# Optimization experiments

Hardware: AMD Instinct MI355X
Metric: run time of the kernel (lower is better)

The kernel has to match this reference:

```python
import jax, jax.numpy as jnp
import numpy as np

HEADS = 8
EPS = 1e-6
LN_EPS = 1e-5


def avg_pool(x, k):
    b, c, h, w = x.shape
    return x.reshape(b, c, h // k, k, w // k, k).mean(axis=(3, 5))


def layernorm(x, g, b):
    mu = x.mean(-1, keepdims=True)
    var = x.var(-1, keepdims=True)
    return (x - mu) / jnp.sqrt(var + LN_EPS) * g + b


def pos_embed_2d(h, w, c):
    # original calls build_2d_sincos_position_embedding(w=h, h=w): grid over (h, w), row-major flatten
    gw, gh = jnp.meshgrid(jnp.arange(h, dtype=jnp.float32),
                          jnp.arange(w, dtype=jnp.float32), indexing='ij')
    pd = c // 4
    omega = 1.0 / (10000.0 ** (jnp.arange(pd, dtype=jnp.float32) / pd))
    ow = gw.reshape(-1, 1) * omega  # (h*w, pd)
    oh = gh.reshape(-1, 1) * omega
    return jnp.concatenate([jnp.sin(ow), jnp.cos(ow), jnp.sin(oh), jnp.cos(oh)], axis=1)  # (h*w, c)


def _forward(a3, a4, q_w, q_b, q_ln_g, q_ln_b, k_w, k_b, k_ln_g, k_ln_b,
             v_w, v_b, out_w, out_b, lin1_w, lin1_b, lin2_w, lin2_b,
             n1_g, n1_b, n2_g, n2_b, idx):
    orig_a3 = a3
    if idx == 2:
        a3d = avg_pool(a3, 2)
    else:
        a3d = avg_pool(a3, 4)
        a4 = avg_pool(a4, 2)
    bs, c, h, w = a3d.shape
    L = h * w  # tgt_len == src_len (a3_down and a4 have equal spatial size)
    hd = c // HEADS

    residual = a3d.reshape(bs, c, L).transpose(0, 2, 1)  # (b, L, c)
    x3 = residual
    x4 = a4.reshape(bs, c, L).transpose(0, 2, 1)
    pos = pos_embed_2d(h, w, c)  # (L, c)
    x3 = x3 + pos[None]
    x4 = x4 + pos[None]

    Q = layernorm(x3 @ q_w + q_b, q_ln_g, q_ln_b)
    K = layernorm(x4 @ k_w + k_b, k_ln_g, k_ln_b)
    V = x4 @ v_w + v_b
    Q = jax.nn.relu(Q).reshape(bs, L, HEADS, hd).transpose(0, 2, 1, 3)  # (b,h,L,d)
    K = jax.nn.relu(K).reshape(bs, L, HEADS, hd).transpose(0, 2, 1, 3)
    V = V.reshape(bs, L, HEADS, hd).transpose(0, 2, 1, 3)

    # cosFormer position reweighting: index = pi/2 * (1..m) / m
    m = L
    wi = (np.pi / 2.0) * jnp.arange(1, m + 1, dtype=jnp.float32) / m  # (m,)
    sn = jnp.sin(wi)[None, None, :, None]
    cs = jnp.cos(wi)[None, None, :, None]
    Q_ = jnp.concatenate([Q * sn, Q * cs], axis=-1)  # (b,h,L,2d)
    K_ = jnp.concatenate([K * sn, K * cs], axis=-1)

    KV = jnp.einsum('bhld,bhlm->bhdm', K_, V)                     # (b,h,2d,d)
    Z = 1.0 / jnp.maximum(jnp.einsum('bhld,bhd->bhl', Q_, K_.sum(axis=2)), EPS)
    attn = jnp.einsum('bhld,bhdm->bhlm', Q_, KV) * Z[..., None]   # (b,h,L,d)
    attn = attn.transpose(0, 2, 1, 3).reshape(bs, L, c)

    out = attn @ out_w + out_b
    out = layernorm(out, n1_g, n1_b)     # normalize_before=False -> norm1 applied
    out = residual + out                 # dropout=0
    res2 = out
    out = jax.nn.gelu(out @ lin1_w + lin1_b, approximate=False) @ lin2_w + lin2_b
    out = layernorm(out, n2_g, n2_b)
    out = res2 + out

    a3sa = out.transpose(0, 2, 1).reshape(bs, c, h, w)
    a3sa = jax.image.resize(a3sa, orig_a3.shape, method='bilinear')  # align_corners=False
    return a3sa * orig_a3


def setup_inputs() -> dict:
    key = jax.random.key(0)
    ks = jax.random.split(key, 10)
    B, C = 16, 256
    C4 = 4 * C

    def w(k, shp):
        return jax.random.normal(k, shp, dtype=jnp.float32) * 0.02

    return {
        'a3': jax.random.normal(ks[0], (B, C, 128, 128), dtype=jnp.float32),
        'a4': jax.random.normal(ks[1], (B, C, 64, 64), dtype=jnp.float32),
        'q_w': w(ks[2], (C, C)), 'q_b': jnp.zeros((C,), jnp.float32),
        'q_ln_g': jnp.ones((C,), jnp.float32), 'q_ln_b': jnp.zeros((C,), jnp.float32),
        'k_w': w(ks[3], (C, C)), 'k_b': jnp.zeros((C,), jnp.float32),
        'k_ln_g': jnp.ones((C,), jnp.float32), 'k_ln_b': jnp.zeros((C,), jnp.float32),
        'v_w': w(ks[4], (C, C)), 'v_b': jnp.zeros((C,), jnp.float32),
        'out_w': w(ks[5], (C, C)), 'out_b': jnp.zeros((C,), jnp.float32),
        'lin1_w': w(ks[6], (C, C4)), 'lin1_b': jnp.zeros((C4,), jnp.float32),
        'lin2_w': w(ks[7], (C4, C)), 'lin2_b': jnp.zeros((C,), jnp.float32),
        'n1_g': jnp.ones((C,), jnp.float32), 'n1_b': jnp.zeros((C,), jnp.float32),
        'n2_g': jnp.ones((C,), jnp.float32), 'n2_b': jnp.zeros((C,), jnp.float32),
        'idx': 2,
    }


def reference(a3, a4, q_w, q_b, q_ln_g, q_ln_b, k_w, k_b, k_ln_g, k_ln_b,
              v_w, v_b, out_w, out_b, lin1_w, lin1_b, lin2_w, lin2_b,
              n1_g, n1_b, n2_g, n2_b, idx):
    return _forward(a3, a4, q_w, q_b, q_ln_g, q_ln_b, k_w, k_b, k_ln_g, k_ln_b,
                    v_w, v_b, out_w, out_b, lin1_w, lin1_b, lin2_w, lin2_b,
                    n1_g, n1_b, n2_g, n2_b, idx)
```

## Files before the change

kernel.cpp:

```cpp
#include <hip/hip_runtime.h>
#include <hip/hip_bf16.h>
#include <math.h>

#define HEADS 8
#define LL 4096
#define CDIM 256
#define BATCH 16
#define NROWS (BATCH*LL)

typedef __attribute__((ext_vector_type(8))) __bf16 bf16x8;
typedef __attribute__((ext_vector_type(4))) float f32x4;

__device__ inline float b2f(ushort u) {
    union { unsigned u; float f; } v; v.u = ((unsigned)u) << 16; return v.f;
}
__device__ inline ushort f2b(float f) {
    union { float f; unsigned u; } v; v.f = f;
    unsigned r = (v.u + 0x7FFF + ((v.u >> 16) & 1)) >> 16;
    return (ushort)r;
}
__device__ inline void gload16(const void* g, void* l) {
    __builtin_amdgcn_global_load_lds(
        (const __attribute__((address_space(1))) unsigned int*)g,
        (__attribute__((address_space(3))) unsigned int*)l, 16, 0, 0);
}

__global__ __launch_bounds__(256) void prep_kernel(
    float* __restrict__ pos, float* __restrict__ snc,
    const float* __restrict__ q_w, const float* __restrict__ k_w,
    const float* __restrict__ v_w, const float* __restrict__ o_w,
    const float* __restrict__ w1, const float* __restrict__ w2,
    ushort* __restrict__ wqT, ushort* __restrict__ wkT,
    ushort* __restrict__ wvT, ushort* __restrict__ woT,
    ushort* __restrict__ w1T, ushort* __restrict__ w2T)
{
    __shared__ float t[32][33];
    int bid = blockIdx.x;
    int tid = threadIdx.x;
    if (bid < 1024) {
        int c = tid;
        int k = c & 63;
        float omega = expf(-(float)k * (9.210340371976184f / 64.0f));
        #pragma unroll
        for (int i = 0; i < 4; ++i) {
            int l = bid * 4 + i;
            int y = l >> 6, x = l & 63;
            float coord = (c < 128) ? (float)y : (float)x;
            float ang = coord * omega;
            float val = ((c & 127) < 64) ? sinf(ang) : cosf(ang);
            pos[l * CDIM + c] = val;
            if (c < 2) {
                float wi = 1.5707963267948966f * (float)(l + 1) / (float)LL;
                snc[l * 2 + c] = (c == 0) ? sinf(wi) : cosf(wi);
            }
        }
        return;
    }
    int id = bid - 1024;
    const float* W; ushort* Wt; int K, N, kb, nb;
    if (id < 64)       { W = q_w; Wt = wqT; K = 256;  N = 256;  kb = (id & 7) * 32;  nb = (id >> 3) * 32; }
    else if (id < 128) { id -= 64;  W = k_w; Wt = wkT; K = 256;  N = 256;  kb = (id & 7) * 32;  nb = (id >> 3) * 32; }
    else if (id < 192) { id -= 128; W = v_w; Wt = wvT; K = 256;  N = 256;  kb = (id & 7) * 32;  nb = (id >> 3) * 32; }
    else if (id < 256) { id -= 192; W = o_w; Wt = woT; K = 256;  N = 256;  kb = (id & 7) * 32;  nb = (id >> 3) * 32; }
    else if (id < 512) { id -= 256; W = w1;  Wt = w1T; K = 256;  N = 1024; kb = (id & 7) * 32;  nb = (id >> 3) * 32; }
    else               { id -= 512; W = w2;  Wt = w2T; K = 1024; N = 256;  kb = (id & 31) * 32; nb = (id >> 5) * 32; }
    int x = tid & 31, y = tid >> 5;
    #pragma unroll
    for (int i = 0; i < 4; ++i)
        t[y + i * 8][x] = W[(size_t)(kb + y + i * 8) * N + nb + x];
    __syncthreads();
    #pragma unroll
    for (int i = 0; i < 4; ++i) {
        int n = y + i * 8;
        Wt[(size_t)(nb + n) * K + kb + x] = f2b(t[x][n]);
    }
}

__global__ __launch_bounds__(256) void pool_x3_kernel(
    const float* __restrict__ a3, ushort* __restrict__ residual,
    ushort* __restrict__ x3b, const float* __restrict__ pos)
{
    __shared__ float raw[64][128];
    __shared__ float pooled[64][65];
    int i = blockIdx.x, ct = blockIdx.y, b = blockIdx.z;
    int tid = threadIdx.x;
    #pragma unroll
    for (int it = 0; it < 8; ++it) {
        int lin = (it * 256 + tid) * 4;
        int x = lin & 127;
        int cc = lin >> 7;
        size_t base = ((size_t)(b * 256 + ct * 64 + cc) * 128 + 2 * i) * 128 + x;
        float4 v0 = *(const float4*)&a3[base];
        float4 v1 = *(const float4*)&a3[base + 128];
        float4 s = make_float4(v0.x + v1.x, v0.y + v1.y, v0.z + v1.z, v0.w + v1.w);
        *(float4*)&raw[cc][x] = s;
    }
    __syncthreads();
    #pragma unroll
    for (int it = 0; it < 16; ++it) {
        int idx = it * 256 + tid;
        int j = idx & 63, cc = idx >> 6;
        pooled[cc][j] = 0.25f * (raw[cc][2 * j] + raw[cc][2 * j + 1]);
    }
    __syncthreads();
    #pragma unroll
    for (int it = 0; it < 16; ++it) {
        int cc = tid & 63;
        int jj = (tid >> 6) + it * 4;
        float val = pooled[cc][jj];
        int l = i * 64 + jj;
        int c = ct * 64 + cc;
        size_t o = (size_t)(b * LL + l) * CDIM + c;
        residual[o] = f2b(val);
        x3b[o] = f2b(val + pos[l * CDIM + c]);
    }
}

__global__ __launch_bounds__(256) void x4_kernel(
    const float* __restrict__ a4, ushort* __restrict__ x4b, const float* __restrict__ pos)
{
    __shared__ float t2[64][65];
    int y = blockIdx.x, ct = blockIdx.y, b = blockIdx.z, tid = threadIdx.x;
    #pragma unroll
    for (int it = 0; it < 16; ++it) {
        int idx = it * 256 + tid;
        int x = idx & 63, cc = idx >> 6;
        t2[cc][x] = a4[((size_t)(b * 256 + ct * 64 + cc) * 64 + y) * 64 + x];
    }
    __syncthreads();
    #pragma unroll
    for (int it = 0; it < 16; ++it) {
        int cc = tid & 63;
        int xx = (tid >> 6) + it * 4;
        int l = y * 64 + xx, c = ct * 64 + cc;
        x4b[(size_t)(b * LL + l) * CDIM + c] = f2b(t2[cc][xx] + pos[l * CDIM + c]);
    }
}

template<bool DO_LN, bool DO_RELU, bool DO_GELU, bool DO_RES>
__global__ __launch_bounds__(512, 2) void gemm_mfma(
    const ushort* __restrict__ A, const ushort* __restrict__ Wt,
    const float* __restrict__ bias, const float* __restrict__ gam_,
    const float* __restrict__ bet_, const ushort* __restrict__ res,
    ushort* __restrict__ outb, int K, int colsTot)
{
    __shared__ ushort As[128 * 32];
    __shared__ ushort Bs[256 * 32];
    __shared__ float redS[128][4];
    __shared__ float redQ[128][4];
    __shared__ float2 mustd[128];

    const int tid = threadIdx.x;
    const int lane = tid & 63;
    const int wv = tid >> 6;
    const int wr = wv >> 2;
    const int wc = wv & 3;
    const int wvu = __builtin_amdgcn_readfirstlane(wv);
    const int row0 = blockIdx.x * 128;
    const int cb = blockIdx.y * 256;

    const int sr = tid >> 2;
    const int sg = (tid & 3) ^ ((sr >> 1) & 3);
    const ushort* aSrc = A + (size_t)(row0 + sr) * K + sg * 8;
    const ushort* bSrc0 = Wt + (size_t)(cb + sr) * K + sg * 8;
    const ushort* bSrc1 = Wt + (size_t)(cb + 128 + sr) * K + sg * 8;

    const int frSlot = (lane >> 4) ^ (((lane & 15) >> 1) & 3);

    f32x4 acc[4][4] = {};
    for (int kb = 0; kb < K; kb += 32) {
        gload16(aSrc + kb, (char*)&As[0] + wvu * 1024);
        gload16(bSrc0 + kb, (char*)&Bs[0] + wvu * 1024);
        gload16(bSrc1 + kb, (char*)&Bs[0] + 8192 + wvu * 1024);
        __syncthreads();

        bf16x8 af[4], bfr[4];
        #pragma unroll
        for (int f = 0; f < 4; ++f) {
            int r = wr * 64 + f * 16 + (lane & 15);
            af[f] = *(const bf16x8*)&As[r * 32 + frSlot * 8];
            int c = wc * 64 + f * 16 + (lane & 15);
            bfr[f] = *(const bf16x8*)&Bs[c * 32 + frSlot * 8];
        }
        #pragma unroll
        for (int fi = 0; fi < 4; ++fi)
            #pragma unroll
            for (int fj = 0; fj < 4; ++fj)
                acc[fi][fj] = __builtin_amdgcn_mfma_f32_16x16x32_bf16(
                    af[fi], bfr[fj], acc[fi][fj], 0, 0, 0);
        __syncthreads();
    }

    const int cl = lane & 15;
    const int rg = lane >> 4;
    float bia[4], gmv[4], btv[4];
    #pragma unroll
    for (int fj = 0; fj < 4; ++fj) {
        int col = cb + wc * 64 + fj * 16 + cl;
        bia[fj] = bias[col];
        if constexpr (DO_LN) { gmv[fj] = gam_[col]; btv[fj] = bet_[col]; }
    }
    #pragma unroll
    for (int fi = 0; fi < 4; ++fi)
        #pragma unroll
        for (int fj = 0; fj < 4; ++fj)
            #pragma unroll
            for (int j = 0; j < 4; ++j)
                acc[fi][fj][j] += bia[fj];

    if constexpr (DO_LN) {
        #pragma unroll
        for (int fi = 0; fi < 4; ++fi)
            #pragma unroll
            for (int j = 0; j < 4; ++j) {
                float s = acc[fi][0][j] + acc[fi][1][j] + acc[fi][2][j] + acc[fi][3][j];
                float q = acc[fi][0][j] * acc[fi][0][j] + acc[fi][1][j] * acc[fi][1][j]
                        + acc[fi][2][j] * acc[fi][2][j] + acc[fi][3][j] * acc[fi][3][j];
                #pragma unroll
                for (int m = 1; m <= 8; m <<= 1) {
                    s += __shfl_xor(s, m, 64);
                    q += __shfl_xor(q, m, 64);
                }
                if (cl == 0) {
                    int tr = wr * 64 + fi * 16 + rg * 4 + j;
                    redS[tr][wc] = s; redQ[tr][wc] = q;
                }
            }
        __syncthreads();
        if (tid < 128) {
            float s = redS[tid][0] + redS[tid][1] + redS[tid][2] + redS[tid][3];
            float q = redQ[tid][0] + redQ[tid][1] + redQ[tid][2] + redQ[tid][3];
            float mu = s * (1.0f / 256.0f);
            float var = q * (1.0f / 256.0f) - mu * mu;
            mustd[tid] = make_float2(mu, rsqrtf(var + 1e-5f));
        }
        __syncthreads();
        #pragma unroll
        for (int fi = 0; fi < 4; ++fi)
            #pragma unroll
            for (int j = 0; j < 4; ++j) {
                float2 ms = mustd[wr * 64 + fi * 16 + rg * 4 + j];
                #pragma unroll
                for (int fj = 0; fj < 4; ++fj)
                    acc[fi][fj][j] = (acc[fi][fj][j] - ms.x) * ms.y * gmv[fj] + btv[fj];
            }
    }
    if constexpr (DO_RELU) {
        #pragma unroll
        for (int fi = 0; fi < 4; ++fi)
            #pragma unroll
            for (int fj = 0; fj < 4; ++fj)
                #pragma unroll
                for (int j = 0; j < 4; ++j)
                    acc[fi][fj][j] = fmaxf(acc[fi][fj][j], 0.0f);
    }
    if constexpr (DO_GELU) {
        #pragma unroll
        for (int fi = 0; fi < 4; ++fi)
            #pragma unroll
            for (int fj = 0; fj < 4; ++fj)
                #pragma unroll
                for (int j = 0; j < 4; ++j) {
                    float v = acc[fi][fj][j];
                    acc[fi][fj][j] = 0.5f * v * (1.0f + erff(v * 0.7071067811865476f));
                }
    }
    #pragma unroll
    for (int fi = 0; fi < 4; ++fi)
        #pragma unroll
        for (int j = 0; j < 4; ++j) {
            size_t row = row0 + wr * 64 + fi * 16 + rg * 4 + j;
            size_t rbase = row * (size_t)colsTot + cb + wc * 64 + cl;
            #pragma unroll
            for (int fj = 0; fj < 4; ++fj) {
                float v = acc[fi][fj][j];
                if constexpr (DO_RES) v += b2f(res[rbase + fj * 16]);
                outb[rbase + fj * 16] = f2b(v);
            }
        }
}

__global__ __launch_bounds__(256) void ksum_kernel(
    const ushort* __restrict__ Kmat, const float* __restrict__ snc,
    float* __restrict__ kspart)
{
    int ch = blockIdx.x, b = blockIdx.y;
    int c = threadIdx.x;
    int l0 = ch * 512;
    float as = 0.0f, ac = 0.0f;
    for (int i = 0; i < 512; ++i) {
        float k = b2f(Kmat[(size_t)(b * LL + l0 + i) * CDIM + c]);
        as += k * snc[(l0 + i) * 2];
        ac += k * snc[(l0 + i) * 2 + 1];
    }
    kspart[((size_t)(b * 8 + ch) * 2 + 0) * 256 + c] = as;
    kspart[((size_t)(b * 8 + ch) * 2 + 1) * 256 + c] = ac;
}

__global__ __launch_bounds__(256) void kv_kernel(
    const ushort* __restrict__ Kmat, const ushort* __restrict__ Vmat,
    const float* __restrict__ snc, float* __restrict__ kvpart)
{
    __shared__ float Kt[64][36];
    __shared__ float Vt[64][36];
    __shared__ float sns[64], css[64];
    int chunk = blockIdx.x;
    int bh = blockIdx.y;
    int b = bh >> 3, h = bh & 7;
    int tid = threadIdx.x;
    int m = tid & 31;
    int d0 = (tid >> 5) * 4;
    float accs[4] = {}, accc[4] = {};
    int l0chunk = chunk * 512;
    int lrow = tid >> 2;
    int lcol = (tid & 3) * 8;
    for (int sub = 0; sub < 8; ++sub) {
        int l0 = l0chunk + sub * 64;
        {
            size_t gbase = (size_t)(b * LL + l0 + lrow) * CDIM + h * 32 + lcol;
            uint4 kr = *(const uint4*)&Kmat[gbase];
            uint4 vr = *(const uint4*)&Vmat[gbase];
            float* kd = &Kt[lrow][lcol];
            float* vd = &Vt[lrow][lcol];
            kd[0] = b2f((ushort)(kr.x & 0xffff)); kd[1] = b2f((ushort)(kr.x >> 16));
            kd[2] = b2f((ushort)(kr.y & 0xffff)); kd[3] = b2f((ushort)(kr.y >> 16));
            kd[4] = b2f((ushort)(kr.z & 0xffff)); kd[5] = b2f((ushort)(kr.z >> 16));
            kd[6] = b2f((ushort)(kr.w & 0xffff)); kd[7] = b2f((ushort)(kr.w >> 16));
            vd[0] = b2f((ushort)(vr.x & 0xffff)); vd[1] = b2f((ushort)(vr.x >> 16));
            vd[2] = b2f((ushort)(vr.y & 0xffff)); vd[3] = b2f((ushort)(vr.y >> 16));
            vd[4] = b2f((ushort)(vr.z & 0xffff)); vd[5] = b2f((ushort)(vr.z >> 16));
            vd[6] = b2f((ushort)(vr.w & 0xffff)); vd[7] = b2f((ushort)(vr.w >> 16));
        }
        if (tid < 64) { sns[tid] = snc[(l0 + tid) * 2]; css[tid] = snc[(l0 + tid) * 2 + 1]; }
        __syncthreads();
        #pragma unroll 4
        for (int lt = 0; lt < 64; ++lt) {
            float v = Vt[lt][m];
            float vs = v * sns[lt];
            float vc = v * css[lt];
            float4 kd4 = *(const float4*)&Kt[lt][d0];
            accs[0] += kd4.x * vs; accc[0] += kd4.x * vc;
            accs[1] += kd4.y * vs; accc[1] += kd4.y * vc;
            accs[2] += kd4.z * vs; accc[2] += kd4.z * vc;
            accs[3] += kd4.w * vs; accc[3] += kd4.w * vc;
        }
        __syncthreads();
    }
    size_t base = (size_t)(bh * 8 + chunk) * 2048;
    #pragma unroll
    for (int i2 = 0; i2 < 4; ++i2) {
        kvpart[base + (d0 + i2) * 32 + m] = accs[i2];
        kvpart[base + 1024 + (d0 + i2) * 32 + m] = accc[i2];
    }
}

__global__ __launch_bounds__(256) void kvred_kernel(
    const float* __restrict__ kvpart, const float* __restrict__ kspart,
    ushort* __restrict__ Bimg)
{
    int bh = blockIdx.x;
    int b = bh >> 3, h = bh & 7;
    int tid = threadIdx.x;
    for (int e = tid; e < 2560; e += 256) {
        int n = e >> 5;
        int k = e & 31;
        int t = n >> 4, col = n & 15;
        float v = 0.0f;
        if (t < 4) {
            int off = (t >= 2 ? 1024 : 0) + k * 32 + (t & 1) * 16 + col;
            #pragma unroll
            for (int ch = 0; ch < 8; ++ch)
                v += kvpart[(size_t)(bh * 8 + ch) * 2048 + off];
        } else if (col < 2) {
            #pragma unroll
            for (int ch = 0; ch < 8; ++ch)
                v += kspart[((size_t)(b * 8 + ch) * 2 + col) * 256 + h * 32 + k];
        }
        ushort hi = f2b(v);
        ushort lo = f2b(v - b2f(hi));
        Bimg[(size_t)bh * 5120 + n * 32 + k] = hi;
        Bimg[(size_t)bh * 5120 + (80 + n) * 32 + k] = lo;
    }
}

__global__ __launch_bounds__(256, 2) void attn_mfma(
    const ushort* __restrict__ Qmat, const ushort* __restrict__ Bimg,
    const float* __restrict__ snc, ushort* __restrict__ attnOut)
{
    __shared__ ushort Bs[5120];
    int ltile = blockIdx.x, h = blockIdx.y, b = blockIdx.z;
    int bh = b * 8 + h;
    int tid = threadIdx.x;
    int lane = tid & 63;
    int wv = tid >> 6;

    for (int e = tid; e < 640; e += 256)
        *(uint4*)&Bs[e * 8] = *(const uint4*)&Bimg[(size_t)bh * 5120 + e * 8];
    __syncthreads();

    bf16x8 bfr[10];
    #pragma unroll
    for (int tt = 0; tt < 10; ++tt) {
        int row = (tt < 5 ? tt * 16 : 80 + (tt - 5) * 16) + (lane & 15);
        bfr[tt] = *(const bf16x8*)&Bs[row * 32 + (lane >> 4) * 8];
    }
    int lbase = ltile * 256 + wv * 64;
    bf16x8 af[4];
    #pragma unroll
    for (int fi = 0; fi < 4; ++fi) {
        int l = lbase + fi * 16 + (lane & 15);
        af[fi] = *(const bf16x8*)&Qmat[(size_t)(b * LL + l) * CDIM + h * 32 + (lane >> 4) * 8];
    }
    f32x4 acc[4][5] = {};
    #pragma unroll
    for (int fi = 0; fi < 4; ++fi)
        #pragma unroll
        for (int t = 0; t < 5; ++t) {
            acc[fi][t] = __builtin_amdgcn_mfma_f32_16x16x32_bf16(af[fi], bfr[t], acc[fi][t], 0, 0, 0);
            acc[fi][t] = __builtin_amdgcn_mfma_f32_16x16x32_bf16(af[fi], bfr[t + 5], acc[fi][t], 0, 0, 0);
        }

    int zlane = lane & 48;
    int cl = lane & 15;
    #pragma unroll
    for (int fi = 0; fi < 4; ++fi) {
        #pragma unroll
        for (int j = 0; j < 4; ++j) {
            float zraw = acc[fi][4][j];
            float zs = __shfl(zraw, zlane, 64);
            float zc = __shfl(zraw, zlane | 1, 64);
            int l = lbase + fi * 16 + ((lane >> 4) & 3) * 4 + j;
            float sn = snc[l * 2], cs = snc[l * 2 + 1];
            float den = sn * zs + cs * zc;
            float Z = 1.0f / fmaxf(den, 1e-6f);
            float v0 = (sn * acc[fi][0][j] + cs * acc[fi][2][j]) * Z;
            float v1 = (sn * acc[fi][1][j] + cs * acc[fi][3][j]) * Z;
            size_t ob = (size_t)(b * LL + l) * CDIM + h * 32 + cl;
            attnOut[ob] = f2b(v0);
            attnOut[ob + 16] = f2b(v1);
        }
    }
}

__global__ __launch_bounds__(256) void resize_mul_kernel(
    const ushort* __restrict__ ffeat, const float* __restrict__ a3, float* __restrict__ out)
{
    __shared__ float ft[3][64][65];
    int k = blockIdx.x, ct = blockIdx.y, b = blockIdx.z;
    int tid = threadIdx.x;
    for (int it = 0; it < 48; ++it) {
        int e = it * 256 + tid;
        int cc = e & 63;
        int xs = (e >> 6) & 63;
        int ys = e >> 12;
        int ysrc = min(max(k - 1 + ys, 0), 63);
        ft[ys][cc][xs] = b2f(ffeat[(size_t)(b * LL + ysrc * 64 + xs) * CDIM + ct * 64 + cc]);
    }
    __syncthreads();
    int x = tid & 127;
    int half = tid >> 7;
    int y = 2 * k + half;
    int ysA, ysB; float wyA, wyB;
    if (half == 0) { ysA = 0; ysB = 1; wyA = 0.25f; wyB = 0.75f; }
    else           { ysA = 1; ysB = 2; wyA = 0.75f; wyB = 0.25f; }
    int x0; float wx1;
    if ((x & 1) == 0) { x0 = x / 2 - 1; wx1 = 0.75f; }
    else              { x0 = x / 2;     wx1 = 0.25f; }
    int x0c = max(x0, 0);
    int x1c = min(x0 + 1, 63);
    float wx0 = 1.0f - wx1;
    for (int cc = 0; cc < 64; ++cc) {
        float rA = wx0 * ft[ysA][cc][x0c] + wx1 * ft[ysA][cc][x1c];
        float rB = wx0 * ft[ysB][cc][x0c] + wx1 * ft[ysB][cc][x1c];
        float val = wyA * rA + wyB * rB;
        size_t oidx = ((size_t)(b * 256 + ct * 64 + cc) * 128 + y) * 128 + x;
        out[oidx] = val * a3[oidx];
    }
}

extern "C" void kernel_launch(void* const* d_in, const int* in_sizes, int n_in,
                              void* d_out, int out_size, void* d_ws, size_t ws_size,
                              hipStream_t stream)
{
    const float* a3     = (const float*)d_in[0];
    const float* a4     = (const float*)d_in[1];
    const float* q_w    = (const float*)d_in[2];
    const float* q_b    = (const float*)d_in[3];
    const float* q_ln_g = (const float*)d_in[4];
    const float* q_ln_b = (const float*)d_in[5];
    const float* k_w    = (const float*)d_in[6];
    const float* k_b    = (const float*)d_in[7];
    const float* k_ln_g = (const float*)d_in[8];
    const float* k_ln_b = (const float*)d_in[9];
    const float* v_w    = (const float*)d_in[10];
    const float* v_b    = (const float*)d_in[11];
    const float* out_w  = (const float*)d_in[12];
    const float* out_b  = (const float*)d_in[13];
    const float* lin1_w = (const float*)d_in[14];
    const float* lin1_b = (const float*)d_in[15];
    const float* lin2_w = (const float*)d_in[16];
    const float* lin2_b = (const float*)d_in[17];
    const float* n1_g   = (const float*)d_in[18];
    const float* n1_b   = (const float*)d_in[19];
    const float* n2_g   = (const float*)d_in[20];
    const float* n2_b   = (const float*)d_in[21];
    float* out = (float*)d_out;
    char* base = (char*)d_ws;

    const size_t MiB = 1024 * 1024;
    float*  pos      = (float*)(base);
    float*  snc      = (float*)(base + 4 * MiB);
    ushort* wqT      = (ushort*)(base + 4 * MiB + 64 * 1024);
    ushort* wkT      = wqT + 256 * 256;
    ushort* wvT      = wkT + 256 * 256;
    ushort* woT      = wvT + 256 * 256;
    ushort* w1T      = woT + 256 * 256;
    ushort* w2T      = w1T + 1024 * 256;
    ushort* residual = (ushort*)(base + 6 * MiB);
    ushort* x3b      = (ushort*)(base + 38 * MiB);
    ushort* x4b      = (ushort*)(base + 70 * MiB);
    ushort* Qb       = (ushort*)(base + 102 * MiB);
    ushort* Kb       = (ushort*)(base + 134 * MiB);
    ushort* Vb       = (ushort*)(base + 166 * MiB);
    float*  kvp      = (float*)(base + 198 * MiB);
    float*  kspart   = (float*)(base + 206 * MiB);
    ushort* Bimg     = (ushort*)(base + 207 * MiB);
    ushort* h1b      = (ushort*)(base + 209 * MiB);
    ushort* attnb    = x3b;
    ushort* res2b    = x4b;
    ushort* ffeat    = residual;

    prep_kernel<<<1792, 256, 0, stream>>>(pos, snc, q_w, k_w, v_w, out_w, lin1_w, lin2_w,
                                          wqT, wkT, wvT, woT, w1T, w2T);
    pool_x3_kernel<<<dim3(64, 4, 16), 256, 0, stream>>>(a3, residual, x3b, pos);
    x4_kernel<<<dim3(64, 4, 16), 256, 0, stream>>>(a4, x4b, pos);

    gemm_mfma<true, true, false, false><<<dim3(NROWS / 128, 1), 512, 0, stream>>>(
        x3b, wqT, q_b, q_ln_g, q_ln_b, nullptr, Qb, 256, 256);
    gemm_mfma<true, true, false, false><<<dim3(NROWS / 128, 1), 512, 0, stream>>>(
        x4b, wkT, k_b, k_ln_g, k_ln_b, nullptr, Kb, 256, 256);
    gemm_mfma<false, false, false, false><<<dim3(NROWS / 128, 1), 512, 0, stream>>>(
        x4b, wvT, v_b, nullptr, nullptr, nullptr, Vb, 256, 256);

    ksum_kernel<<<dim3(8, 16), 256, 0, stream>>>(Kb, snc, kspart);
    kv_kernel<<<dim3(8, 128), 256, 0, stream>>>(Kb, Vb, snc, kvp);
    kvred_kernel<<<128, 256, 0, stream>>>(kvp, kspart, Bimg);
    attn_mfma<<<dim3(16, 8, 16), 256, 0, stream>>>(Qb, Bimg, snc, attnb);

    gemm_mfma<true, false, false, true><<<dim3(NROWS / 128, 1), 512, 0, stream>>>(
        attnb, woT, out_b, n1_g, n1_b, residual, res2b, 256, 256);
    gemm_mfma<false, false, true, false><<<dim3(NROWS / 128, 4), 512, 0, stream>>>(
        res2b, w1T, lin1_b, nullptr, nullptr, nullptr, h1b, 256, 1024);
    gemm_mfma<true, false, false, true><<<dim3(NROWS / 128, 1), 512, 0, stream>>>(
        h1b, w2T, lin2_b, n2_g, n2_b, res2b, ffeat, 1024, 256);

    resize_mul_kernel<<<dim3(64, 4, 16), 256, 0, stream>>>(ffeat, a3, out);
}
```

Measured before the change: 605.5 us.

## Fuse MLP GEMMs through LDS and double-buffer smaller-tile GEMM kernel

Adds an mlp_fused kernel that computes lin1+GELU into an LDS-resident 64x256 hidden chunk and immediately multiplies it by the matching slice of lin2, accumulating across four chunks before bias, LayerNorm and the residual add. This removes the round trip of the 64x1024 hidden activation through global memory. The generic GEMM is also rewritten to 64-row tiles with 256 threads and double-buffered LDS prefetch of the next K slice, specialised to K=256. In exchange it uses more LDS per block, which lowers occupancy, and each block reloads its A tile once per chunk.

```diff
diff --git a/kernel.cpp b/kernel.cpp
--- a/kernel.cpp
+++ b/kernel.cpp
@@ -137,50 +137,55 @@
     }
 }
 
-template<bool DO_LN, bool DO_RELU, bool DO_GELU, bool DO_RES>
-__global__ __launch_bounds__(512, 2) void gemm_mfma(
+template<bool DO_LN, bool DO_RELU, bool DO_RES>
+__global__ __launch_bounds__(256, 3) void gemm_mfma(
     const ushort* __restrict__ A, const ushort* __restrict__ Wt,
     const float* __restrict__ bias, const float* __restrict__ gam_,
     const float* __restrict__ bet_, const ushort* __restrict__ res,
-    ushort* __restrict__ outb, int K, int colsTot)
-{
-    __shared__ ushort As[128 * 32];
-    __shared__ ushort Bs[256 * 32];
-    __shared__ float redS[128][4];
-    __shared__ float redQ[128][4];
-    __shared__ float2 mustd[128];
+    ushort* __restrict__ outb)
+{
+    __shared__ ushort As[2][64 * 32];
+    __shared__ ushort Bs[2][256 * 32];
+    __shared__ float redS[64][4];
+    __shared__ float redQ[64][4];
+    __shared__ float2 mustd[64];
 
     const int tid = threadIdx.x;
     const int lane = tid & 63;
     const int wv = tid >> 6;
-    const int wr = wv >> 2;
-    const int wc = wv & 3;
     const int wvu = __builtin_amdgcn_readfirstlane(wv);
-    const int row0 = blockIdx.x * 128;
-    const int cb = blockIdx.y * 256;
+    const int row0 = blockIdx.x * 64;
 
     const int sr = tid >> 2;
     const int sg = (tid & 3) ^ ((sr >> 1) & 3);
-    const ushort* aSrc = A + (size_t)(row0 + sr) * K + sg * 8;
-    const ushort* bSrc0 = Wt + (size_t)(cb + sr) * K + sg * 8;
-    const ushort* bSrc1 = Wt + (size_t)(cb + 128 + sr) * K + sg * 8;
+    const ushort* aSrc = A + (size_t)(row0 + sr) * 256 + sg * 8;
+    const ushort* bSrc = Wt + (size_t)sr * 256 + sg * 8;
 
     const int frSlot = (lane >> 4) ^ (((lane & 15) >> 1) & 3);
 
     f32x4 acc[4][4] = {};
-    for (int kb = 0; kb < K; kb += 32) {
-        gload16(aSrc + kb, (char*)&As[0] + wvu * 1024);
-        gload16(bSrc0 + kb, (char*)&Bs[0] + wvu * 1024);
-        gload16(bSrc1 + kb, (char*)&Bs[0] + 8192 + wvu * 1024);
-        __syncthreads();
-
+    gload16(aSrc, (char*)&As[0][0] + wvu * 1024);
+    #pragma unroll
+    for (int j = 0; j < 4; ++j)
+        gload16(bSrc + j * 64 * 256, (char*)&Bs[0][0] + j * 4096 + wvu * 1024);
+    __syncthreads();
+
+    int cur = 0;
+    for (int t = 0; t < 8; ++t) {
+        if (t < 7) {
+            gload16(aSrc + (t + 1) * 32, (char*)&As[cur ^ 1][0] + wvu * 1024);
+            #pragma unroll
+            for (int j = 0; j < 4; ++j)
+                gload16(bSrc + j * 64 * 256 + (t + 1) * 32,
+                        (char*)&Bs[cur ^ 1][0] + j * 4096 + wvu * 1024);
+        }
         bf16x8 af[4], bfr[4];
         #pragma unroll
         for (int f = 0; f < 4; ++f) {
-            int r = wr * 64 + f * 16 + (lane & 15);
-            af[f] = *(const bf16x8*)&As[r * 32 + frSlot * 8];
-            int c = wc * 64 + f * 16 + (lane & 15);
-            bfr[f] = *(const bf16x8*)&Bs[c * 32 + frSlot * 8];
+            int r = f * 16 + (lane & 15);
+            af[f] = *(const bf16x8*)&As[cur][r * 32 + frSlot * 8];
+            int c = wv * 64 + f * 16 + (lane & 15);
+            bfr[f] = *(const bf16x8*)&Bs[cur][c * 32 + frSlot * 8];
         }
         #pragma unroll
         for (int fi = 0; fi < 4; ++fi)
@@ -189,6 +194,7 @@
                 acc[fi][fj] = __builtin_amdgcn_mfma_f32_16x16x32_bf16(
                     af[fi], bfr[fj], acc[fi][fj], 0, 0, 0);
         __syncthreads();
+        cur ^= 1;
     }
 
     const int cl = lane & 15;
@@ -196,7 +202,7 @@
     float bia[4], gmv[4], btv[4];
     #pragma unroll
     for (int fj = 0; fj < 4; ++fj) {
-        int col = cb + wc * 64 + fj * 16 + cl;
+        int col = wv * 64 + fj * 16 + cl;
         bia[fj] = bias[col];
         if constexpr (DO_LN) { gmv[fj] = gam_[col]; btv[fj] = bet_[col]; }
     }
@@ -221,13 +227,10 @@
                     s += __shfl_xor(s, m, 64);
                     q += __shfl_xor(q, m, 64);
                 }
-                if (cl == 0) {
-                    int tr = wr * 64 + fi * 16 + rg * 4 + j;
-                    redS[tr][wc] = s; redQ[tr][wc] = q;
-                }
+                if (cl == 0) { redS[fi * 16 + rg * 4 + j][wv] = s; redQ[fi * 16 + rg * 4 + j][wv] = q; }
             }
         __syncthreads();
-        if (tid < 128) {
+        if (tid < 64) {
             float s = redS[tid][0] + redS[tid][1] + redS[tid][2] + redS[tid][3];
             float q = redQ[tid][0] + redQ[tid][1] + redQ[tid][2] + redQ[tid][3];
             float mu = s * (1.0f / 256.0f);
@@ -239,7 +242,7 @@
         for (int fi = 0; fi < 4; ++fi)
             #pragma unroll
             for (int j = 0; j < 4; ++j) {
-                float2 ms = mustd[wr * 64 + fi * 16 + rg * 4 + j];
+                float2 ms = mustd[fi * 16 + rg * 4 + j];
                 #pragma unroll
                 for (int fj = 0; fj < 4; ++fj)
                     acc[fi][fj][j] = (acc[fi][fj][j] - ms.x) * ms.y * gmv[fj] + btv[fj];
@@ -254,27 +257,180 @@
                 for (int j = 0; j < 4; ++j)
                     acc[fi][fj][j] = fmaxf(acc[fi][fj][j], 0.0f);
     }
-    if constexpr (DO_GELU) {
+    #pragma unroll
+    for (int fi = 0; fi < 4; ++fi)
+        #pragma unroll
+        for (int j = 0; j < 4; ++j) {
+            size_t row = row0 + fi * 16 + rg * 4 + j;
+            size_t rbase = row * 256 + wv * 64 + cl;
+            #pragma unroll
+            for (int fj = 0; fj < 4; ++fj) {
+                float v = acc[fi][fj][j];
+                if constexpr (DO_RES) v += b2f(res[rbase + fj * 16]);
+                outb[rbase + fj * 16] = f2b(v);
+            }
+        }
+}
+
+__global__ __launch_bounds__(256, 2) void mlp_fused(
+    const ushort* __restrict__ res2, const ushort* __restrict__ w1T,
+    const ushort* __restrict__ w2T, const float* __restrict__ b1,
+    const float* __restrict__ b2, const float* __restrict__ gam_,
+    const float* __restrict__ bet_, ushort* __restrict__ outb)
+{
+    __shared__ ushort As[2][64 * 32];
+    __shared__ ushort Bs[2][256 * 32];
+    __shared__ ushort h1c[64 * 256];
+    __shared__ float redS[64][4];
+    __shared__ float redQ[64][4];
+    __shared__ float2 mustd[64];
+
+    const int tid = threadIdx.x;
+    const int lane = tid & 63;
+    const int wv = tid >> 6;
+    const int wvu = __builtin_amdgcn_readfirstlane(wv);
+    const int row0 = blockIdx.x * 64;
+    const int sr = tid >> 2;
+    const int sg = (tid & 3) ^ ((sr >> 1) & 3);
+    const ushort* aSrc = res2 + (size_t)(row0 + sr) * 256 + sg * 8;
+    const int frSlot = (lane >> 4) ^ (((lane & 15) >> 1) & 3);
+    const int cl = lane & 15;
+    const int rg = lane >> 4;
+
+    f32x4 acc2[4][4] = {};
+    for (int c = 0; c < 4; ++c) {
+        const ushort* b1Src = w1T + (size_t)(c * 256 + sr) * 256 + sg * 8;
+        f32x4 acc1[4][4] = {};
+        gload16(aSrc, (char*)&As[0][0] + wvu * 1024);
+        #pragma unroll
+        for (int j = 0; j < 4; ++j)
+            gload16(b1Src + j * 64 * 256, (char*)&Bs[0][0] + j * 4096 + wvu * 1024);
+        __syncthreads();
+        int cur = 0;
+        for (int t = 0; t < 8; ++t) {
+            if (t < 7) {
+                gload16(aSrc + (t + 1) * 32, (char*)&As[cur ^ 1][0] + wvu * 1024);
+                #pragma unroll
+                for (int j = 0; j < 4; ++j)
+                    gload16(b1Src + j * 64 * 256 + (t + 1) * 32,
+                            (char*)&Bs[cur ^ 1][0] + j * 4096 + wvu * 1024);
+            }
+            bf16x8 af[4], bfr[4];
+            #pragma unroll
+            for (int f = 0; f < 4; ++f) {
+                int r = f * 16 + (lane & 15);
+                af[f] = *(const bf16x8*)&As[cur][r * 32 + frSlot * 8];
+                int cc2 = wv * 64 + f * 16 + (lane & 15);
+                bfr[f] = *(const bf16x8*)&Bs[cur][cc2 * 32 + frSlot * 8];
+            }
+            #pragma unroll
+            for (int fi = 0; fi < 4; ++fi)
+                #pragma unroll
+                for (int fj = 0; fj < 4; ++fj)
+                    acc1[fi][fj] = __builtin_amdgcn_mfma_f32_16x16x32_bf16(
+                        af[fi], bfr[fj], acc1[fi][fj], 0, 0, 0);
+            __syncthreads();
+            cur ^= 1;
+        }
+        float bia1[4];
+        #pragma unroll
+        for (int fj = 0; fj < 4; ++fj)
+            bia1[fj] = b1[c * 256 + wv * 64 + fj * 16 + cl];
         #pragma unroll
         for (int fi = 0; fi < 4; ++fi)
             #pragma unroll
             for (int fj = 0; fj < 4; ++fj)
                 #pragma unroll
                 for (int j = 0; j < 4; ++j) {
-                    float v = acc[fi][fj][j];
-                    acc[fi][fj][j] = 0.5f * v * (1.0f + erff(v * 0.7071067811865476f));
+                    float v = acc1[fi][fj][j] + bia1[fj];
+                    float g = 0.5f * v * (1.0f + erff(v * 0.7071067811865476f));
+                    int row = fi * 16 + rg * 4 + j;
+                    int kk = wv * 64 + fj * 16 + cl;
+                    int s_ = kk >> 5, gg = (kk >> 3) & 3, e = kk & 7;
+                    int slot = gg ^ ((row >> 1) & 3);
+                    h1c[row * 256 + s_ * 32 + slot * 8 + e] = f2b(g);
                 }
+        __syncthreads();
+        const ushort* b2Src = w2T + (size_t)sr * 1024 + c * 256 + sg * 8;
+        #pragma unroll
+        for (int j = 0; j < 4; ++j)
+            gload16(b2Src + (size_t)j * 64 * 1024, (char*)&Bs[0][0] + j * 4096 + wvu * 1024);
+        __syncthreads();
+        cur = 0;
+        for (int t = 0; t < 8; ++t) {
+            if (t < 7) {
+                #pragma unroll
+                for (int j = 0; j < 4; ++j)
+                    gload16(b2Src + (size_t)j * 64 * 1024 + (t + 1) * 32,
+                            (char*)&Bs[cur ^ 1][0] + j * 4096 + wvu * 1024);
+            }
+            bf16x8 af[4], bfr[4];
+            #pragma unroll
+            for (int f = 0; f < 4; ++f) {
+                int r = f * 16 + (lane & 15);
+                af[f] = *(const bf16x8*)&h1c[r * 256 + t * 32 + frSlot * 8];
+                int cc2 = wv * 64 + f * 16 + (lane & 15);
+                bfr[f] = *(const bf16x8*)&Bs[cur][cc2 * 32 + frSlot * 8];
+            }
+            #pragma unroll
+            for (int fi = 0; fi < 4; ++fi)
+                #pragma unroll
+                for (int fj = 0; fj < 4; ++fj)
+                    acc2[fi][fj] = __builtin_amdgcn_mfma_f32_16x16x32_bf16(
+                        af[fi], bfr[fj], acc2[fi][fj], 0, 0, 0);
+            __syncthreads();
+            cur ^= 1;
+        }
+    }
+    float bia[4], gmv[4], btv[4];
+    #pragma unroll
+    for (int fj = 0; fj < 4; ++fj) {
+        int col = wv * 64 + fj * 16 + cl;
+        bia[fj] = b2[col];
+        gmv[fj] = gam_[col];
+        btv[fj] = bet_[col];
     }
     #pragma unroll
     for (int fi = 0; fi < 4; ++fi)
         #pragma unroll
+        for (int fj = 0; fj < 4; ++fj)
+            #pragma unroll
+            for (int j = 0; j < 4; ++j)
+                acc2[fi][fj][j] += bia[fj];
+    #pragma unroll
+    for (int fi = 0; fi < 4; ++fi)
+        #pragma unroll
         for (int j = 0; j < 4; ++j) {
-            size_t row = row0 + wr * 64 + fi * 16 + rg * 4 + j;
-            size_t rbase = row * (size_t)colsTot + cb + wc * 64 + cl;
+            float s = acc2[fi][0][j] + acc2[fi][1][j] + acc2[fi][2][j] + acc2[fi][3][j];
+            float q = acc2[fi][0][j] * acc2[fi][0][j] + acc2[fi][1][j] * acc2[fi][1][j]
+                    + acc2[fi][2][j] * acc2[fi][2][j] + acc2[fi][3][j] * acc2[fi][3][j];
+            #pragma unroll
+            for (int m = 1; m <= 8; m <<= 1) {
+                s += __shfl_xor(s, m, 64);
+                q += __shfl_xor(q, m, 64);
+            }
+            if (cl == 0) { redS[fi * 16 + rg * 4 + j][wv] = s; redQ[fi * 16 + rg * 4 + j][wv] = q; }
+        }
+    __syncthreads();
+    if (tid < 64) {
+        float s = redS[tid][0] + redS[tid][1] + redS[tid][2] + redS[tid][3];
+        float q = redQ[tid][0] + redQ[tid][1] + redQ[tid][2] + redQ[tid][3];
+        float mu = s * (1.0f / 256.0f);
+        float var = q * (1.0f / 256.0f) - mu * mu;
+        mustd[tid] = make_float2(mu, rsqrtf(var + 1e-5f));
+    }
+    __syncthreads();
+    #pragma unroll
+    for (int fi = 0; fi < 4; ++fi)
+        #pragma unroll
+        for (int j = 0; j < 4; ++j) {
+            float2 ms = mustd[fi * 16 + rg * 4 + j];
+            size_t row = row0 + fi * 16 + rg * 4 + j;
+            size_t rbase = row * 256 + wv * 64 + cl;
             #pragma unroll
             for (int fj = 0; fj < 4; ++fj) {
-                float v = acc[fi][fj][j];
-                if constexpr (DO_RES) v += b2f(res[rbase + fj * 16]);
+                float v = (acc2[fi][fj][j] - ms.x) * ms.y * gmv[fj] + btv[fj];
+                v += b2f(res2[rbase + fj * 16]);
                 outb[rbase + fj * 16] = f2b(v);
             }
         }
@@ -525,7 +681,6 @@
     float*  kvp      = (float*)(base + 198 * MiB);
     float*  kspart   = (float*)(base + 206 * MiB);
     ushort* Bimg     = (ushort*)(base + 207 * MiB);
-    ushort* h1b      = (ushort*)(base + 209 * MiB);
     ushort* attnb    = x3b;
     ushort* res2b    = x4b;
     ushort* ffeat    = residual;
@@ -535,24 +690,22 @@
     pool_x3_kernel<<<dim3(64, 4, 16), 256, 0, stream>>>(a3, residual, x3b, pos);
     x4_kernel<<<dim3(64, 4, 16), 256, 0, stream>>>(a4, x4b, pos);
 
-    gemm_mfma<true, true, false, false><<<dim3(NROWS / 128, 1), 512, 0, stream>>>(
-        x3b, wqT, q_b, q_ln_g, q_ln_b, nullptr, Qb, 256, 256);
-    gemm_mfma<true, true, false, false><<<dim3(NROWS / 128, 1), 512, 0, stream>>>(
-        x4b, wkT, k_b, k_ln_g, k_ln_b, nullptr, Kb, 256, 256);
-    gemm_mfma<false, false, false, false><<<dim3(NROWS / 128, 1), 512, 0, stream>>>(
-        x4b, wvT, v_b, nullptr, nullptr, nullptr, Vb, 256, 256);
+    gemm_mfma<true, true, false><<<NROWS / 64, 256, 0, stream>>>(
+        x3b, wqT, q_b, q_ln_g, q_ln_b, nullptr, Qb);
+    gemm_mfma<true, true, false><<<NROWS / 64, 256, 0, stream>>>(
+        x4b, wkT, k_b, k_ln_g, k_ln_b, nullptr, Kb);
+    gemm_mfma<false, false, false><<<NROWS / 64, 256, 0, stream>>>(
+        x4b, wvT, v_b, nullptr, nullptr, nullptr, Vb);
 
     ksum_kernel<<<dim3(8, 16), 256, 0, stream>>>(Kb, snc, kspart);
     kv_kernel<<<dim3(8, 128), 256, 0, stream>>>(Kb, Vb, snc, kvp);
     kvred_kernel<<<128, 256, 0, stream>>>(kvp, kspart, Bimg);
     attn_mfma<<<dim3(16, 8, 16), 256, 0, stream>>>(Qb, Bimg, snc, attnb);
 
-    gemm_mfma<true, false, false, true><<<dim3(NROWS / 128, 1), 512, 0, stream>>>(
-        attnb, woT, out_b, n1_g, n1_b, residual, res2b, 256, 256);
-    gemm_mfma<false, false, true, false><<<dim3(NROWS / 128, 4), 512, 0, stream>>>(
-        res2b, w1T, lin1_b, nullptr, nullptr, nullptr, h1b, 256, 1024);
-    gemm_mfma<true, false, false, true><<<dim3(NROWS / 128, 1), 512, 0, stream>>>(
-        h1b, w2T, lin2_b, n2_g, n2_b, res2b, ffeat, 1024, 256);
+    gemm_mfma<true, false, true><<<NROWS / 64, 256, 0, stream>>>(
+        attnb, woT, out_b, n1_g, n1_b, residual, res2b);
+    mlp_fused<<<NROWS / 64, 256, 0, stream>>>(
+        res2b, w1T, w2T, lin1_b, lin2_b, n2_g, n2_b, ffeat);
 
     resize_mul_kernel<<<dim3(64, 4, 16), 256, 0, stream>>>(ffeat, a3, out);
 }
```

New measurement: 608.8 us. Within noise of the previous version (+0.5%).

## Triple-buffer GEMM K-loop, fuse K-sum into K projection, use tanh GELU

Applied to the files above, without the earlier changes.

The GEMM main loop now uses three LDS buffers with asynchronous global-to-LDS prefetch two steps ahead and vmcnt waits, replacing the two full barriers per K-step. This aims to overlap load latency with MFMA work. The separate ksum kernel is removed: the K-projection GEMM epilogue accumulates sin/cos-weighted column sums and atomically adds them into a zeroed global buffer. The GELU uses a tanh approximation in place of erf, which saves transcendental cost but changes numerics slightly. LDS use triples, which may reduce occupancy.

```diff
diff --git a/kernel.cpp b/kernel.cpp
--- a/kernel.cpp
+++ b/kernel.cpp
@@ -23,6 +23,15 @@
     __builtin_amdgcn_global_load_lds(
         (const __attribute__((address_space(1))) unsigned int*)g,
         (__attribute__((address_space(3))) unsigned int*)l, 16, 0, 0);
+}
+template<int N> __device__ inline void wait_vmcnt() {
+    asm volatile("s_waitcnt vmcnt(%0)" :: "n"(N) : "memory");
+}
+__device__ inline float fast_gelu(float v) {
+    float u = 0.7978845608028654f * v * (1.0f + 0.044715f * v * v);
+    float e = exp2f(u * 2.885390081777927f);
+    float t = 1.0f - 2.0f / (e + 1.0f);
+    return 0.5f * v * (1.0f + t);
 }
 
 __global__ __launch_bounds__(256) void prep_kernel(
@@ -32,11 +41,16 @@
     const float* __restrict__ w1, const float* __restrict__ w2,
     ushort* __restrict__ wqT, ushort* __restrict__ wkT,
     ushort* __restrict__ wvT, ushort* __restrict__ woT,
-    ushort* __restrict__ w1T, ushort* __restrict__ w2T)
+    ushort* __restrict__ w1T, ushort* __restrict__ w2T,
+    float* __restrict__ ksglob)
 {
     __shared__ float t[32][33];
     int bid = blockIdx.x;
     int tid = threadIdx.x;
+    if (bid == 1792) {
+        for (int i = tid; i < BATCH * 2 * 256; i += 256) ksglob[i] = 0.0f;
+        return;
+    }
     if (bid < 1024) {
         int c = tid;
         int k = c & 63;
@@ -137,15 +151,17 @@
     }
 }
 
-template<bool DO_LN, bool DO_RELU, bool DO_GELU, bool DO_RES>
+template<int KSTEPS, bool DO_LN, bool DO_RELU, bool DO_GELU, bool DO_RES, bool DO_KSUM>
 __global__ __launch_bounds__(512, 2) void gemm_mfma(
     const ushort* __restrict__ A, const ushort* __restrict__ Wt,
     const float* __restrict__ bias, const float* __restrict__ gam_,
     const float* __restrict__ bet_, const ushort* __restrict__ res,
-    ushort* __restrict__ outb, int K, int colsTot)
-{
-    __shared__ ushort As[128 * 32];
-    __shared__ ushort Bs[256 * 32];
+    const float* __restrict__ snc, float* __restrict__ ksglob,
+    ushort* __restrict__ outb, int colsTot)
+{
+    constexpr int K = KSTEPS * 32;
+    __shared__ ushort As[3][128 * 32];
+    __shared__ ushort Bs[3][256 * 32];
     __shared__ float redS[128][4];
     __shared__ float redQ[128][4];
     __shared__ float2 mustd[128];
@@ -157,30 +173,37 @@
     const int wc = wv & 3;
     const int wvu = __builtin_amdgcn_readfirstlane(wv);
     const int row0 = blockIdx.x * 128;
-    const int cb = blockIdx.y * 256;
+    const int cbBase = blockIdx.y * 256;
 
     const int sr = tid >> 2;
     const int sg = (tid & 3) ^ ((sr >> 1) & 3);
     const ushort* aSrc = A + (size_t)(row0 + sr) * K + sg * 8;
-    const ushort* bSrc0 = Wt + (size_t)(cb + sr) * K + sg * 8;
-    const ushort* bSrc1 = Wt + (size_t)(cb + 128 + sr) * K + sg * 8;
+    const ushort* bSrc0 = Wt + (size_t)(cbBase + sr) * K + sg * 8;
+    const ushort* bSrc1 = Wt + (size_t)(cbBase + 128 + sr) * K + sg * 8;
 
     const int frSlot = (lane >> 4) ^ (((lane & 15) >> 1) & 3);
 
+    auto issue = [&](int t, int buf) {
+        gload16(aSrc + t * 32, (char*)&As[buf][0] + wvu * 1024);
+        gload16(bSrc0 + t * 32, (char*)&Bs[buf][0] + wvu * 1024);
+        gload16(bSrc1 + t * 32, (char*)&Bs[buf][0] + 8192 + wvu * 1024);
+    };
+
     f32x4 acc[4][4] = {};
-    for (int kb = 0; kb < K; kb += 32) {
-        gload16(aSrc + kb, (char*)&As[0] + wvu * 1024);
-        gload16(bSrc0 + kb, (char*)&Bs[0] + wvu * 1024);
-        gload16(bSrc1 + kb, (char*)&Bs[0] + 8192 + wvu * 1024);
-        __syncthreads();
-
+    issue(0, 0); issue(1, 1);
+    #pragma unroll
+    for (int t = 0; t < KSTEPS; ++t) {
+        if (t < KSTEPS - 1) wait_vmcnt<3>(); else wait_vmcnt<0>();
+        __builtin_amdgcn_s_barrier();
+        if (t + 2 < KSTEPS) issue(t + 2, (t + 2) % 3);
+        const int cb = t % 3;
         bf16x8 af[4], bfr[4];
         #pragma unroll
         for (int f = 0; f < 4; ++f) {
             int r = wr * 64 + f * 16 + (lane & 15);
-            af[f] = *(const bf16x8*)&As[r * 32 + frSlot * 8];
+            af[f] = *(const bf16x8*)&As[cb][r * 32 + frSlot * 8];
             int c = wc * 64 + f * 16 + (lane & 15);
-            bfr[f] = *(const bf16x8*)&Bs[c * 32 + frSlot * 8];
+            bfr[f] = *(const bf16x8*)&Bs[cb][c * 32 + frSlot * 8];
         }
         #pragma unroll
         for (int fi = 0; fi < 4; ++fi)
@@ -188,15 +211,15 @@
             for (int fj = 0; fj < 4; ++fj)
                 acc[fi][fj] = __builtin_amdgcn_mfma_f32_16x16x32_bf16(
                     af[fi], bfr[fj], acc[fi][fj], 0, 0, 0);
-        __syncthreads();
-    }
+    }
+    __syncthreads();
 
     const int cl = lane & 15;
     const int rg = lane >> 4;
     float bia[4], gmv[4], btv[4];
     #pragma unroll
     for (int fj = 0; fj < 4; ++fj) {
-        int col = cb + wc * 64 + fj * 16 + cl;
+        int col = cbBase + wc * 64 + fj * 16 + cl;
         bia[fj] = bias[col];
         if constexpr (DO_LN) { gmv[fj] = gam_[col]; btv[fj] = bet_[col]; }
     }
@@ -260,41 +283,44 @@
             #pragma unroll
             for (int fj = 0; fj < 4; ++fj)
                 #pragma unroll
-                for (int j = 0; j < 4; ++j) {
-                    float v = acc[fi][fj][j];
-                    acc[fi][fj][j] = 0.5f * v * (1.0f + erff(v * 0.7071067811865476f));
-                }
-    }
+                for (int j = 0; j < 4; ++j)
+                    acc[fi][fj][j] = fast_gelu(acc[fi][fj][j]);
+    }
+    float kss[4] = {}, ksc[4] = {};
     #pragma unroll
     for (int fi = 0; fi < 4; ++fi)
         #pragma unroll
         for (int j = 0; j < 4; ++j) {
-            size_t row = row0 + wr * 64 + fi * 16 + rg * 4 + j;
-            size_t rbase = row * (size_t)colsTot + cb + wc * 64 + cl;
+            int rloc = wr * 64 + fi * 16 + rg * 4 + j;
+            size_t row = row0 + rloc;
+            size_t rbase = row * (size_t)colsTot + cbBase + wc * 64 + cl;
+            float sn, cs;
+            if constexpr (DO_KSUM) {
+                int l = (int)(row & (LL - 1));
+                sn = snc[l * 2]; cs = snc[l * 2 + 1];
+            }
             #pragma unroll
             for (int fj = 0; fj < 4; ++fj) {
                 float v = acc[fi][fj][j];
                 if constexpr (DO_RES) v += b2f(res[rbase + fj * 16]);
                 outb[rbase + fj * 16] = f2b(v);
+                if constexpr (DO_KSUM) { kss[fj] += sn * v; ksc[fj] += cs * v; }
             }
         }
-}
-
-__global__ __launch_bounds__(256) void ksum_kernel(
-    const ushort* __restrict__ Kmat, const float* __restrict__ snc,
-    float* __restrict__ kspart)
-{
-    int ch = blockIdx.x, b = blockIdx.y;
-    int c = threadIdx.x;
-    int l0 = ch * 512;
-    float as = 0.0f, ac = 0.0f;
-    for (int i = 0; i < 512; ++i) {
-        float k = b2f(Kmat[(size_t)(b * LL + l0 + i) * CDIM + c]);
-        as += k * snc[(l0 + i) * 2];
-        ac += k * snc[(l0 + i) * 2 + 1];
-    }
-    kspart[((size_t)(b * 8 + ch) * 2 + 0) * 256 + c] = as;
-    kspart[((size_t)(b * 8 + ch) * 2 + 1) * 256 + c] = ac;
+    if constexpr (DO_KSUM) {
+        int b = row0 >> 12;
+        #pragma unroll
+        for (int fj = 0; fj < 4; ++fj) {
+            float s = kss[fj], c = ksc[fj];
+            s += __shfl_xor(s, 16, 64); s += __shfl_xor(s, 32, 64);
+            c += __shfl_xor(c, 16, 64); c += __shfl_xor(c, 32, 64);
+            if (rg == 0) {
+                int col = wc * 64 + fj * 16 + cl;
+                atomicAdd(&ksglob[((size_t)b * 2 + 0) * 256 + col], s);
+                atomicAdd(&ksglob[((size_t)b * 2 + 1) * 256 + col], c);
+            }
+        }
+    }
 }
 
 __global__ __launch_bounds__(256) void kv_kernel(
@@ -355,7 +381,7 @@
 }
 
 __global__ __launch_bounds__(256) void kvred_kernel(
-    const float* __restrict__ kvpart, const float* __restrict__ kspart,
+    const float* __restrict__ kvpart, const float* __restrict__ ksglob,
     ushort* __restrict__ Bimg)
 {
     int bh = blockIdx.x;
@@ -372,9 +398,7 @@
             for (int ch = 0; ch < 8; ++ch)
                 v += kvpart[(size_t)(bh * 8 + ch) * 2048 + off];
         } else if (col < 2) {
-            #pragma unroll
-            for (int ch = 0; ch < 8; ++ch)
-                v += kspart[((size_t)(b * 8 + ch) * 2 + col) * 256 + h * 32 + k];
+            v = ksglob[((size_t)b * 2 + col) * 256 + h * 32 + k];
         }
         ushort hi = f2b(v);
         ushort lo = f2b(v - b2f(hi));
@@ -523,36 +547,35 @@
     ushort* Kb       = (ushort*)(base + 134 * MiB);
     ushort* Vb       = (ushort*)(base + 166 * MiB);
     float*  kvp      = (float*)(base + 198 * MiB);
-    float*  kspart   = (float*)(base + 206 * MiB);
+    float*  ksglob   = (float*)(base + 206 * MiB);
     ushort* Bimg     = (ushort*)(base + 207 * MiB);
     ushort* h1b      = (ushort*)(base + 209 * MiB);
     ushort* attnb    = x3b;
     ushort* res2b    = x4b;
     ushort* ffeat    = residual;
 
-    prep_kernel<<<1792, 256, 0, stream>>>(pos, snc, q_w, k_w, v_w, out_w, lin1_w, lin2_w,
-                                          wqT, wkT, wvT, woT, w1T, w2T);
+    prep_kernel<<<1793, 256, 0, stream>>>(pos, snc, q_w, k_w, v_w, out_w, lin1_w, lin2_w,
+                                          wqT, wkT, wvT, woT, w1T, w2T, ksglob);
     pool_x3_kernel<<<dim3(64, 4, 16), 256, 0, stream>>>(a3, residual, x3b, pos);
     x4_kernel<<<dim3(64, 4, 16), 256, 0, stream>>>(a4, x4b, pos);
 
-    gemm_mfma<true, true, false, false><<<dim3(NROWS / 128, 1), 512, 0, stream>>>(
-        x3b, wqT, q_b, q_ln_g, q_ln_b, nullptr, Qb, 256, 256);
-    gemm_mfma<true, true, false, false><<<dim3(NROWS / 128, 1), 512, 0, stream>>>(
-        x4b, wkT, k_b, k_ln_g, k_ln_b, nullptr, Kb, 256, 256);
-    gemm_mfma<false, false, false, false><<<dim3(NROWS / 128, 1), 512, 0, stream>>>(
-        x4b, wvT, v_b, nullptr, nullptr, nullptr, Vb, 256, 256);
-
-    ksum_kernel<<<dim3(8, 16), 256, 0, stream>>>(Kb, snc, kspart);
+    gemm_mfma<8, true, true, false, false, false><<<dim3(NROWS / 128, 1), 512, 0, stream>>>(
+        x3b, wqT, q_b, q_ln_g, q_ln_b, nullptr, nullptr, nullptr, Qb, 256);
+    gemm_mfma<8, true, true, false, false, true><<<dim3(NROWS / 128, 1), 512, 0, stream>>>(
+        x4b, wkT, k_b, k_ln_g, k_ln_b, nullptr, snc, ksglob, Kb, 256);
+    gemm_mfma<8, false, false, false, false, false><<<dim3(NROWS / 128, 1), 512, 0, stream>>>(
+        x4b, wvT, v_b, nullptr, nullptr, nullptr, nullptr, nullptr, Vb, 256);
+
     kv_kernel<<<dim3(8, 128), 256, 0, stream>>>(Kb, Vb, snc, kvp);
-    kvred_kernel<<<128, 256, 0, stream>>>(kvp, kspart, Bimg);
+    kvred_kernel<<<128, 256, 0, stream>>>(kvp, ksglob, Bimg);
     attn_mfma<<<dim3(16, 8, 16), 256, 0, stream>>>(Qb, Bimg, snc, attnb);
 
-    gemm_mfma<true, false, false, true><<<dim3(NROWS / 128, 1), 512, 0, stream>>>(
-        attnb, woT, out_b, n1_g, n1_b, residual, res2b, 256, 256);
-    gemm_mfma<false, false, true, false><<<dim3(NROWS / 128, 4), 512, 0, stream>>>(
-        res2b, w1T, lin1_b, nullptr, nullptr, nullptr, h1b, 256, 1024);
-    gemm_mfma<true, false, false, true><<<dim3(NROWS / 128, 1), 512, 0, stream>>>(
-        h1b, w2T, lin2_b, n2_g, n2_b, res2b, ffeat, 1024, 256);
+    gemm_mfma<8, true, false, false, true, false><<<dim3(NROWS / 128, 1), 512, 0, stream>>>(
+        attnb, woT, out_b, n1_g, n1_b, residual, nullptr, nullptr, res2b, 256);
+    gemm_mfma<8, false, false, true, false, false><<<dim3(NROWS / 128, 4), 512, 0, stream>>>(
+        res2b, w1T, lin1_b, nullptr, nullptr, nullptr, nullptr, nullptr, h1b, 1024);
+    gemm_mfma<32, true, false, false, true, false><<<dim3(NROWS / 128, 1), 512, 0, stream>>>(
+        h1b, w2T, lin2_b, n2_g, n2_b, res2b, nullptr, nullptr, ffeat, 256);
 
     resize_mul_kernel<<<dim3(64, 4, 16), 256, 0, stream>>>(ffeat, a3, out);
 }
```

Measured after the change: 587.3 us. -3.0%, faster.
